# Kernel optimization log

Hardware: AMD Instinct MI355X
Metric: run time of the kernel (lower is better)

Reference implementation:

```python
import jax, jax.numpy as jnp
import numpy as np

N_HEAD = 8
N_FEAT = 512
D_HEAD = N_FEAT // N_HEAD


def setup_inputs() -> dict:
    key = jax.random.key(0)
    ks = jax.random.split(key, 11)
    B, T, L = 4, 2048, 16
    s = 1.0 / np.sqrt(D_HEAD)
    so = 1.0 / np.sqrt(N_FEAT)
    return {
        "q": jax.random.normal(ks[0], (B, T, 1, N_FEAT), jnp.float32),
        "k": jax.random.normal(ks[1], (B, T, L, N_FEAT), jnp.float32),
        "v": jax.random.normal(ks[2], (B, T, L, N_FEAT), jnp.float32),
        "Wq": jax.random.uniform(ks[3], (D_HEAD, D_HEAD), jnp.float32, -s, s),
        "bq": jax.random.uniform(ks[4], (D_HEAD,), jnp.float32, -s, s),
        "Wk": jax.random.uniform(ks[5], (D_HEAD, D_HEAD), jnp.float32, -s, s),
        "bk": jax.random.uniform(ks[6], (D_HEAD,), jnp.float32, -s, s),
        "Wv": jax.random.uniform(ks[7], (D_HEAD, D_HEAD), jnp.float32, -s, s),
        "bv": jax.random.uniform(ks[8], (D_HEAD,), jnp.float32, -s, s),
        "Wo": jax.random.uniform(ks[9], (N_FEAT, N_FEAT), jnp.float32, -so, so),
        "bo": jax.random.uniform(ks[10], (N_FEAT,), jnp.float32, -so, so),
    }


def reference(q, k, v, Wq, bq, Wk, bk, Wv, bv, Wo, bo):
    B, T, L, F = k.shape
    H, D = N_HEAD, D_HEAD
    # split heads: q [B,T,H,D] (query axis of length 1 squeezed), k/v [B,T,L,H,D]
    qh = q.reshape(B, T, H, D)
    kh = k.reshape(B, T, L, H, D)
    vh = v.reshape(B, T, L, H, D)
    # per-head linear projections (shared across heads), Linear: x @ W^T + b
    qh = jnp.einsum("bthd,ed->bthe", qh, Wq) + bq
    kh = jnp.einsum("btlhd,ed->btlhe", kh, Wk) + bk
    vh = jnp.einsum("btlhd,ed->btlhe", vh, Wv) + bv
    # attention scores over the local window L (query length 1 per timestep)
    attw = jnp.einsum("bthd,btlhd->bthl", qh, kh) / jnp.sqrt(jnp.asarray(D, qh.dtype))
    attn = jax.nn.softmax(attw, axis=-1)  # dropout is identity in eval mode
    ct = jnp.einsum("bthl,btlhd->bthd", attn, vh)
    ct = ct.reshape(B, T, F)
    return ct @ Wo.T + bo
```

## Files before the change

kernel.cpp:

```cpp
#include <hip/hip_runtime.h>


#define NFEAT 512
#define NHEAD 8
#define DHEAD 64
#define LWIN  16
#define WPOS  8
#define FBT   16
#define VPITCH 520

typedef __attribute__((ext_vector_type(8))) short bf16x8;
typedef __attribute__((ext_vector_type(4))) float f32x4;

__device__ __forceinline__ unsigned short f2bf(float f) {
    unsigned int u = __float_as_uint(f);
    unsigned int r = (u + 0x7fffu + ((u >> 16) & 1u)) >> 16;
    return (unsigned short)r;
}

__global__ void precompute_small(const float* __restrict__ Wq, const float* __restrict__ bq,
                                 const float* __restrict__ Wk,
                                 const float* __restrict__ Wo, const float* __restrict__ bo,
                                 const float* __restrict__ bv,
                                 float* __restrict__ A, float* __restrict__ g,
                                 float* __restrict__ b2) {
    int idx = blockIdx.x * 256 + threadIdx.x;
    if (idx < 4096) {
        int d = idx >> 6, dp = idx & 63;
        float s = 0.f;
        #pragma unroll 8
        for (int e = 0; e < 64; ++e) s = fmaf(Wq[e * 64 + d], Wk[e * 64 + dp], s);
        A[idx] = s;
    } else if (idx < 4160) {
        int dp = idx - 4096;
        float s = 0.f;
        #pragma unroll 8
        for (int e = 0; e < 64; ++e) s = fmaf(Wk[e * 64 + dp], bq[e], s);
        g[dp] = s;
    } else if (idx < 4672) {
        int j = idx - 4160;
        float s = bo[j];
        #pragma unroll 8
        for (int i = 0; i < 512; ++i) s = fmaf(Wo[j * 512 + i], bv[i & 63], s);
        b2[j] = s;
    }
}

__global__ void precompute_wo2(const float* __restrict__ Wo, const float* __restrict__ Wv,
                               unsigned short* __restrict__ Wo2B) {
    int idx = blockIdx.x * 256 + threadIdx.x;
    int i = idx & 511, j = idx >> 9;
    int h = i >> 6, e = i & 63;
    float s = 0.f;
    #pragma unroll 8
    for (int d = 0; d < 64; ++d)
        s = fmaf(Wo[j * 512 + h * 64 + d], Wv[d * 64 + e], s);
    Wo2B[(size_t)j * 512 + i] = f2bf(s);
}

__global__ __launch_bounds__(512, 4)
void w_prepass(const float* __restrict__ q, const float* __restrict__ A,
               const float* __restrict__ g, float* __restrict__ Wm) {
    __shared__ float As[4096];
    __shared__ float qs[WPOS][NFEAT];
    const int tid = threadIdx.x;
    const int bt0 = blockIdx.x * WPOS;

    #pragma unroll
    for (int i = 0; i < 8; ++i) As[i * 512 + tid] = A[i * 512 + tid];
    #pragma unroll
    for (int r = 0; r < WPOS; ++r) qs[r][tid] = q[(size_t)(bt0 + r) * NFEAT + tid];
    __syncthreads();

    const int e  = tid & 63;
    const int hb = (tid >> 6) << 6;
    float acc[WPOS];
    const float ge = g[e];
    #pragma unroll
    for (int r = 0; r < WPOS; ++r) acc[r] = ge;

    #pragma unroll 4
    for (int dq = 0; dq < 16; ++dq) {
        const float a0 = As[(4 * dq + 0) * 64 + e];
        const float a1 = As[(4 * dq + 1) * 64 + e];
        const float a2 = As[(4 * dq + 2) * 64 + e];
        const float a3 = As[(4 * dq + 3) * 64 + e];
        #pragma unroll
        for (int r = 0; r < WPOS; ++r) {
            const float4 qv = *reinterpret_cast<const float4*>(&qs[r][hb + 4 * dq]);
            acc[r] = fmaf(qv.x, a0, acc[r]);
            acc[r] = fmaf(qv.y, a1, acc[r]);
            acc[r] = fmaf(qv.z, a2, acc[r]);
            acc[r] = fmaf(qv.w, a3, acc[r]);
        }
    }
    #pragma unroll
    for (int r = 0; r < WPOS; ++r)
        Wm[(size_t)(bt0 + r) * NFEAT + tid] = acc[r] * 0.125f;
}

__global__ __launch_bounds__(512, 4)
void attn_fused(const float* __restrict__ Wm, const float* __restrict__ k,
                const float* __restrict__ v, const unsigned short* __restrict__ Wo2B,
                const float* __restrict__ b2, float* __restrict__ out) {
    __shared__ float ps[NHEAD][FBT][17];
    __shared__ __align__(16) unsigned char uni[FBT * NFEAT * 4];
    float*          wsT   = reinterpret_cast<float*>(uni);
    unsigned short* vbarS = reinterpret_cast<unsigned short*>(uni);

    const int tid = threadIdx.x;
    const int bt0 = blockIdx.x * FBT;

    #pragma unroll 4
    for (int r = 0; r < FBT; ++r)
        wsT[r * NFEAT + tid] = Wm[(size_t)(bt0 + r) * NFEAT + tid];
    __syncthreads();

    {
        const int h    = tid >> 6;
        const int lane = tid & 63;
        const int l    = lane >> 2;
        const int d4   = lane & 3;
        #pragma unroll 4
        for (int pp = 0; pp < FBT; ++pp) {
            const float4* w4 = reinterpret_cast<const float4*>(
                wsT + pp * NFEAT + h * 64 + d4 * 16);
            const float4* k4 = reinterpret_cast<const float4*>(
                k + (size_t)(bt0 + pp) * (LWIN * NFEAT) + (size_t)l * NFEAT + h * 64 + d4 * 16);
            float a0 = 0.f, a1 = 0.f, a2 = 0.f, a3 = 0.f;
            #pragma unroll
            for (int i = 0; i < 4; ++i) {
                const float4 wq = w4[i];
                const float4 kq = k4[i];
                a0 = fmaf(wq.x, kq.x, a0);
                a1 = fmaf(wq.y, kq.y, a1);
                a2 = fmaf(wq.z, kq.z, a2);
                a3 = fmaf(wq.w, kq.w, a3);
            }
            float sc = (a0 + a1) + (a2 + a3);
            sc += __shfl_xor(sc, 1, 64);
            sc += __shfl_xor(sc, 2, 64);
            const float e = __expf(sc);
            float s = e;
            s += __shfl_xor(s, 4, 64);
            s += __shfl_xor(s, 8, 64);
            s += __shfl_xor(s, 16, 64);
            s += __shfl_xor(s, 32, 64);
            if (d4 == 0) ps[h][pp][l] = e * (1.0f / s);
        }
    }
    __syncthreads();

    {
        const int pb = tid >> 7;
        const int f4 = tid & 127;
        const int hh = f4 >> 4;
        #pragma unroll
        for (int ii = 0; ii < 4; ++ii) {
            const int bt = ii * 4 + pb;
            float pv[LWIN];
            #pragma unroll
            for (int i = 0; i < LWIN; ++i) pv[i] = ps[hh][bt][i];
            const float4* vp = reinterpret_cast<const float4*>(
                v + (size_t)(bt0 + bt) * (LWIN * NFEAT)) + f4;
            float ax = 0.f, ay = 0.f, az = 0.f, aw = 0.f;
            #pragma unroll
            for (int l = 0; l < LWIN; ++l) {
                const float4 vv = vp[(size_t)l * 128];
                ax = fmaf(pv[l], vv.x, ax);
                ay = fmaf(pv[l], vv.y, ay);
                az = fmaf(pv[l], vv.z, az);
                aw = fmaf(pv[l], vv.w, aw);
            }
            unsigned short o[4] = { f2bf(ax), f2bf(ay), f2bf(az), f2bf(aw) };
            *reinterpret_cast<uint2*>(vbarS + bt * VPITCH + f4 * 4) =
                *reinterpret_cast<uint2*>(o);
        }
    }
    __syncthreads();

    {
        const int w    = tid >> 6;
        const int lane = tid & 63;
        const int n0   = w * 64;
        const int r    = lane & 15;
        const int kg   = lane >> 4;

        const unsigned short* As0 = vbarS + r * VPITCH + kg * 8;
        const short* Bb0 = (const short*)Wo2B + ((size_t)(n0 +  0 + r)) * 512 + kg * 8;
        const short* Bb1 = (const short*)Wo2B + ((size_t)(n0 + 16 + r)) * 512 + kg * 8;
        const short* Bb2 = (const short*)Wo2B + ((size_t)(n0 + 32 + r)) * 512 + kg * 8;
        const short* Bb3 = (const short*)Wo2B + ((size_t)(n0 + 48 + r)) * 512 + kg * 8;

        f32x4 acc0 = {0.f, 0.f, 0.f, 0.f}, acc1 = acc0, acc2 = acc0, acc3 = acc0;

        #pragma unroll 4
        for (int kk = 0; kk < 16; ++kk) {
            const bf16x8 a   = *reinterpret_cast<const bf16x8*>(As0 + kk * 32);
            const bf16x8 b0  = *reinterpret_cast<const bf16x8*>(Bb0 + kk * 32);
            const bf16x8 b1  = *reinterpret_cast<const bf16x8*>(Bb1 + kk * 32);
            const bf16x8 b2v = *reinterpret_cast<const bf16x8*>(Bb2 + kk * 32);
            const bf16x8 b3  = *reinterpret_cast<const bf16x8*>(Bb3 + kk * 32);
            acc0 = __builtin_amdgcn_mfma_f32_16x16x32_bf16(a, b0,  acc0, 0, 0, 0);
            acc1 = __builtin_amdgcn_mfma_f32_16x16x32_bf16(a, b1,  acc1, 0, 0, 0);
            acc2 = __builtin_amdgcn_mfma_f32_16x16x32_bf16(a, b2v, acc2, 0, 0, 0);
            acc3 = __builtin_amdgcn_mfma_f32_16x16x32_bf16(a, b3,  acc3, 0, 0, 0);
        }

        const float bb0 = b2[n0 + 0 + r],  bb1 = b2[n0 + 16 + r];
        const float bb2 = b2[n0 + 32 + r], bb3 = b2[n0 + 48 + r];
        #pragma unroll
        for (int j = 0; j < 4; ++j) {
            const size_t row = (size_t)(bt0 + kg * 4 + j) * 512;
            out[row + n0 +  0 + r] = acc0[j] + bb0;
            out[row + n0 + 16 + r] = acc1[j] + bb1;
            out[row + n0 + 32 + r] = acc2[j] + bb2;
            out[row + n0 + 48 + r] = acc3[j] + bb3;
        }
    }
}

extern "C" void kernel_launch(void* const* d_in, const int* in_sizes, int n_in,
                              void* d_out, int out_size, void* d_ws, size_t ws_size,
                              hipStream_t stream) {
    const float* q  = (const float*)d_in[0];
    const float* k  = (const float*)d_in[1];
    const float* v  = (const float*)d_in[2];
    const float* Wq = (const float*)d_in[3];
    const float* bq = (const float*)d_in[4];
    const float* Wk = (const float*)d_in[5];
    const float* Wv = (const float*)d_in[7];
    const float* bv = (const float*)d_in[8];
    const float* Wo = (const float*)d_in[9];
    const float* bo = (const float*)d_in[10];
    float* out = (float*)d_out;

    float* ws = (float*)d_ws;
    float*          A    = ws;
    float*          g    = ws + 4096;
    float*          b2   = ws + 4160;
    unsigned short* Wo2B = (unsigned short*)(ws + 4672);
    float*          Wm   = ws + 4672 + 131072;

    const int BT = in_sizes[0] / NFEAT;

    hipLaunchKernelGGL(precompute_small, dim3(19), dim3(256), 0, stream,
                       Wq, bq, Wk, Wo, bo, bv, A, g, b2);
    hipLaunchKernelGGL(precompute_wo2, dim3(1024), dim3(256), 0, stream,
                       Wo, Wv, Wo2B);
    hipLaunchKernelGGL(w_prepass, dim3(BT / WPOS), dim3(512), 0, stream,
                       q, A, g, Wm);
    hipLaunchKernelGGL(attn_fused, dim3(BT / FBT), dim3(512), 0, stream,
                       Wm, k, v, Wo2B, b2, out);
}
```

Baseline: 174.9 us.

## Read Wm directly from global and batch loads ahead of FMAs with sched barriers

Drops the LDS staging of the Wm tile and its barrier, reading the per-position query-projected weights straight from global memory in the score phase. Scores are now processed two timesteps at a time, and both the score and V-weighting phases issue all their global loads before a sched_barrier, so more memory requests are in flight before the arithmetic starts. This removes a shared-memory round trip and one sync and shrinks LDS use to the bf16 vbar buffer only. In exchange, register pressure rises under the 512-thread, 4-block launch bound, which can lead to spills, and the outer V loop is no longer unrolled.

```diff
diff --git a/kernel.cpp b/kernel.cpp
--- a/kernel.cpp
+++ b/kernel.cpp
@@ -99,79 +99,133 @@
         Wm[(size_t)(bt0 + r) * NFEAT + tid] = acc[r] * 0.125f;
 }
 
+__device__ __forceinline__ void dot4x4(const float4 w0, const float4 w1,
+                                       const float4 w2, const float4 w3,
+                                       const float4 k0, const float4 k1,
+                                       const float4 k2, const float4 k3,
+                                       float& outv) {
+    float a0 = 0.f, a1 = 0.f, a2 = 0.f, a3 = 0.f;
+    a0 = fmaf(w0.x, k0.x, a0); a1 = fmaf(w0.y, k0.y, a1);
+    a2 = fmaf(w0.z, k0.z, a2); a3 = fmaf(w0.w, k0.w, a3);
+    a0 = fmaf(w1.x, k1.x, a0); a1 = fmaf(w1.y, k1.y, a1);
+    a2 = fmaf(w1.z, k1.z, a2); a3 = fmaf(w1.w, k1.w, a3);
+    a0 = fmaf(w2.x, k2.x, a0); a1 = fmaf(w2.y, k2.y, a1);
+    a2 = fmaf(w2.z, k2.z, a2); a3 = fmaf(w2.w, k2.w, a3);
+    a0 = fmaf(w3.x, k3.x, a0); a1 = fmaf(w3.y, k3.y, a1);
+    a2 = fmaf(w3.z, k3.z, a2); a3 = fmaf(w3.w, k3.w, a3);
+    outv = (a0 + a1) + (a2 + a3);
+}
+
 __global__ __launch_bounds__(512, 4)
 void attn_fused(const float* __restrict__ Wm, const float* __restrict__ k,
                 const float* __restrict__ v, const unsigned short* __restrict__ Wo2B,
                 const float* __restrict__ b2, float* __restrict__ out) {
     __shared__ float ps[NHEAD][FBT][17];
-    __shared__ __align__(16) unsigned char uni[FBT * NFEAT * 4];
-    float*          wsT   = reinterpret_cast<float*>(uni);
-    unsigned short* vbarS = reinterpret_cast<unsigned short*>(uni);
+    __shared__ __align__(16) unsigned short vbarS[FBT * VPITCH];
 
     const int tid = threadIdx.x;
     const int bt0 = blockIdx.x * FBT;
-
-    #pragma unroll 4
-    for (int r = 0; r < FBT; ++r)
-        wsT[r * NFEAT + tid] = Wm[(size_t)(bt0 + r) * NFEAT + tid];
-    __syncthreads();
 
     {
         const int h    = tid >> 6;
         const int lane = tid & 63;
         const int l    = lane >> 2;
         const int d4   = lane & 3;
-        #pragma unroll 4
-        for (int pp = 0; pp < FBT; ++pp) {
-            const float4* w4 = reinterpret_cast<const float4*>(
-                wsT + pp * NFEAT + h * 64 + d4 * 16);
-            const float4* k4 = reinterpret_cast<const float4*>(
-                k + (size_t)(bt0 + pp) * (LWIN * NFEAT) + (size_t)l * NFEAT + h * 64 + d4 * 16);
-            float a0 = 0.f, a1 = 0.f, a2 = 0.f, a3 = 0.f;
-            #pragma unroll
-            for (int i = 0; i < 4; ++i) {
-                const float4 wq = w4[i];
-                const float4 kq = k4[i];
-                a0 = fmaf(wq.x, kq.x, a0);
-                a1 = fmaf(wq.y, kq.y, a1);
-                a2 = fmaf(wq.z, kq.z, a2);
-                a3 = fmaf(wq.w, kq.w, a3);
+        const int off  = h * 64 + d4 * 16;
+
+        for (int pp2 = 0; pp2 < FBT / 2; ++pp2) {
+            const int pa = 2 * pp2, pb = 2 * pp2 + 1;
+            const float4* wA = reinterpret_cast<const float4*>(
+                Wm + (size_t)(bt0 + pa) * NFEAT + off);
+            const float4* wB = reinterpret_cast<const float4*>(
+                Wm + (size_t)(bt0 + pb) * NFEAT + off);
+            const float4* kA = reinterpret_cast<const float4*>(
+                k + (size_t)(bt0 + pa) * (LWIN * NFEAT) + (size_t)l * NFEAT + off);
+            const float4* kB = reinterpret_cast<const float4*>(
+                k + (size_t)(bt0 + pb) * (LWIN * NFEAT) + (size_t)l * NFEAT + off);
+
+            const float4 wa0 = wA[0], wa1 = wA[1], wa2 = wA[2], wa3 = wA[3];
+            const float4 ka0 = kA[0], ka1 = kA[1], ka2 = kA[2], ka3 = kA[3];
+            const float4 wb0 = wB[0], wb1 = wB[1], wb2 = wB[2], wb3 = wB[3];
+            const float4 kb0 = kB[0], kb1 = kB[1], kb2 = kB[2], kb3 = kB[3];
+            __builtin_amdgcn_sched_barrier(0);
+
+            float sa, sb;
+            dot4x4(wa0, wa1, wa2, wa3, ka0, ka1, ka2, ka3, sa);
+            dot4x4(wb0, wb1, wb2, wb3, kb0, kb1, kb2, kb3, sb);
+
+            sa += __shfl_xor(sa, 1, 64);  sb += __shfl_xor(sb, 1, 64);
+            sa += __shfl_xor(sa, 2, 64);  sb += __shfl_xor(sb, 2, 64);
+            const float ea = __expf(sa);  const float eb = __expf(sb);
+            float da = ea, db = eb;
+            da += __shfl_xor(da, 4, 64);  db += __shfl_xor(db, 4, 64);
+            da += __shfl_xor(da, 8, 64);  db += __shfl_xor(db, 8, 64);
+            da += __shfl_xor(da, 16, 64); db += __shfl_xor(db, 16, 64);
+            da += __shfl_xor(da, 32, 64); db += __shfl_xor(db, 32, 64);
+            if (d4 == 0) {
+                ps[h][pa][l] = ea * (1.0f / da);
+                ps[h][pb][l] = eb * (1.0f / db);
             }
-            float sc = (a0 + a1) + (a2 + a3);
-            sc += __shfl_xor(sc, 1, 64);
-            sc += __shfl_xor(sc, 2, 64);
-            const float e = __expf(sc);
-            float s = e;
-            s += __shfl_xor(s, 4, 64);
-            s += __shfl_xor(s, 8, 64);
-            s += __shfl_xor(s, 16, 64);
-            s += __shfl_xor(s, 32, 64);
-            if (d4 == 0) ps[h][pp][l] = e * (1.0f / s);
         }
     }
     __syncthreads();
 
     {
-        const int pb = tid >> 7;
+        const int pq = tid >> 7;
         const int f4 = tid & 127;
         const int hh = f4 >> 4;
-        #pragma unroll
         for (int ii = 0; ii < 4; ++ii) {
-            const int bt = ii * 4 + pb;
+            const int bt = ii * 4 + pq;
             float pv[LWIN];
             #pragma unroll
             for (int i = 0; i < LWIN; ++i) pv[i] = ps[hh][bt][i];
             const float4* vp = reinterpret_cast<const float4*>(
                 v + (size_t)(bt0 + bt) * (LWIN * NFEAT)) + f4;
+
+            const float4 x0  = vp[ 0 * 128], x1  = vp[ 1 * 128];
+            const float4 x2  = vp[ 2 * 128], x3  = vp[ 3 * 128];
+            const float4 x4  = vp[ 4 * 128], x5  = vp[ 5 * 128];
+            const float4 x6  = vp[ 6 * 128], x7  = vp[ 7 * 128];
+            const float4 x8  = vp[ 8 * 128], x9  = vp[ 9 * 128];
+            const float4 x10 = vp[10 * 128], x11 = vp[11 * 128];
+            const float4 x12 = vp[12 * 128], x13 = vp[13 * 128];
+            const float4 x14 = vp[14 * 128], x15 = vp[15 * 128];
+            __builtin_amdgcn_sched_barrier(0);
+
             float ax = 0.f, ay = 0.f, az = 0.f, aw = 0.f;
-            #pragma unroll
-            for (int l = 0; l < LWIN; ++l) {
-                const float4 vv = vp[(size_t)l * 128];
-                ax = fmaf(pv[l], vv.x, ax);
-                ay = fmaf(pv[l], vv.y, ay);
-                az = fmaf(pv[l], vv.z, az);
-                aw = fmaf(pv[l], vv.w, aw);
-            }
+            ax = fmaf(pv[ 0], x0.x,  ax); ay = fmaf(pv[ 0], x0.y,  ay);
+            az = fmaf(pv[ 0], x0.z,  az); aw = fmaf(pv[ 0], x0.w,  aw);
+            ax = fmaf(pv[ 1], x1.x,  ax); ay = fmaf(pv[ 1], x1.y,  ay);
+            az = fmaf(pv[ 1], x1.z,  az); aw = fmaf(pv[ 1], x1.w,  aw);
+            ax = fmaf(pv[ 2], x2.x,  ax); ay = fmaf(pv[ 2], x2.y,  ay);
+            az = fmaf(pv[ 2], x2.z,  az); aw = fmaf(pv[ 2], x2.w,  aw);
+            ax = fmaf(pv[ 3], x3.x,  ax); ay = fmaf(pv[ 3], x3.y,  ay);
+            az = fmaf(pv[ 3], x3.z,  az); aw = fmaf(pv[ 3], x3.w,  aw);
+            ax = fmaf(pv[ 4], x4.x,  ax); ay = fmaf(pv[ 4], x4.y,  ay);
+            az = fmaf(pv[ 4], x4.z,  az); aw = fmaf(pv[ 4], x4.w,  aw);
+            ax = fmaf(pv[ 5], x5.x,  ax); ay = fmaf(pv[ 5], x5.y,  ay);
+            az = fmaf(pv[ 5], x5.z,  az); aw = fmaf(pv[ 5], x5.w,  aw);
+            ax = fmaf(pv[ 6], x6.x,  ax); ay = fmaf(pv[ 6], x6.y,  ay);
+            az = fmaf(pv[ 6], x6.z,  az); aw = fmaf(pv[ 6], x6.w,  aw);
+            ax = fmaf(pv[ 7], x7.x,  ax); ay = fmaf(pv[ 7], x7.y,  ay);
+            az = fmaf(pv[ 7], x7.z,  az); aw = fmaf(pv[ 7], x7.w,  aw);
+            ax = fmaf(pv[ 8], x8.x,  ax); ay = fmaf(pv[ 8], x8.y,  ay);
+            az = fmaf(pv[ 8], x8.z,  az); aw = fmaf(pv[ 8], x8.w,  aw);
+            ax = fmaf(pv[ 9], x9.x,  ax); ay = fmaf(pv[ 9], x9.y,  ay);
+            az = fmaf(pv[ 9], x9.z,  az); aw = fmaf(pv[ 9], x9.w,  aw);
+            ax = fmaf(pv[10], x10.x, ax); ay = fmaf(pv[10], x10.y, ay);
+            az = fmaf(pv[10], x10.z, az); aw = fmaf(pv[10], x10.w, aw);
+            ax = fmaf(pv[11], x11.x, ax); ay = fmaf(pv[11], x11.y, ay);
+            az = fmaf(pv[11], x11.z, az); aw = fmaf(pv[11], x11.w, aw);
+            ax = fmaf(pv[12], x12.x, ax); ay = fmaf(pv[12], x12.y, ay);
+            az = fmaf(pv[12], x12.z, az); aw = fmaf(pv[12], x12.w, aw);
+            ax = fmaf(pv[13], x13.x, ax); ay = fmaf(pv[13], x13.y, ay);
+            az = fmaf(pv[13], x13.z, az); aw = fmaf(pv[13], x13.w, aw);
+            ax = fmaf(pv[14], x14.x, ax); ay = fmaf(pv[14], x14.y, ay);
+            az = fmaf(pv[14], x14.z, az); aw = fmaf(pv[14], x14.w, aw);
+            ax = fmaf(pv[15], x15.x, ax); ay = fmaf(pv[15], x15.y, ay);
+            az = fmaf(pv[15], x15.z, az); aw = fmaf(pv[15], x15.w, aw);
+
             unsigned short o[4] = { f2bf(ax), f2bf(ay), f2bf(az), f2bf(aw) };
             *reinterpret_cast<uint2*>(vbarS + bt * VPITCH + f4 * 4) =
                 *reinterpret_cast<uint2*>(o);
```

New measurement: 181.2 us. +3.6%, slower.

## Halve rows per block, drop Wm LDS staging, defer softmax normalization

Applied to the files above, without the earlier changes.

Cuts the timesteps per block from 16 to 8 and removes the shared-memory staging of the projected query rows, which are now read straight from global memory. This shrinks LDS use so the launch bound can ask for 8 blocks per CU. The softmax sum is no longer a cross-lane shuffle reduction; it is computed per thread from the stored exponentials and applied after the value accumulation. The MFMA tile still uses 16 rows, so half its work is redundant (rows 8-15 duplicate 0-7) and those outputs are not stored, and the Wo weights are reloaded twice as often per output row.

```diff
diff --git a/kernel.cpp b/kernel.cpp
--- a/kernel.cpp
+++ b/kernel.cpp
@@ -6,7 +6,7 @@
 #define DHEAD 64
 #define LWIN  16
 #define WPOS  8
-#define FBT   16
+#define FBT   8
 #define VPITCH 520
 
 typedef __attribute__((ext_vector_type(8))) short bf16x8;
@@ -99,34 +99,28 @@
         Wm[(size_t)(bt0 + r) * NFEAT + tid] = acc[r] * 0.125f;
 }
 
-__global__ __launch_bounds__(512, 4)
+__global__ __launch_bounds__(512, 8)
 void attn_fused(const float* __restrict__ Wm, const float* __restrict__ k,
                 const float* __restrict__ v, const unsigned short* __restrict__ Wo2B,
                 const float* __restrict__ b2, float* __restrict__ out) {
     __shared__ float ps[NHEAD][FBT][17];
-    __shared__ __align__(16) unsigned char uni[FBT * NFEAT * 4];
-    float*          wsT   = reinterpret_cast<float*>(uni);
-    unsigned short* vbarS = reinterpret_cast<unsigned short*>(uni);
+    __shared__ __align__(16) unsigned short vbarS[FBT * VPITCH];
 
     const int tid = threadIdx.x;
     const int bt0 = blockIdx.x * FBT;
-
-    #pragma unroll 4
-    for (int r = 0; r < FBT; ++r)
-        wsT[r * NFEAT + tid] = Wm[(size_t)(bt0 + r) * NFEAT + tid];
-    __syncthreads();
 
     {
         const int h    = tid >> 6;
         const int lane = tid & 63;
         const int l    = lane >> 2;
         const int d4   = lane & 3;
-        #pragma unroll 4
-        for (int pp = 0; pp < FBT; ++pp) {
+        const int off  = h * 64 + d4 * 16;
+
+        for (int p = 0; p < FBT; ++p) {
             const float4* w4 = reinterpret_cast<const float4*>(
-                wsT + pp * NFEAT + h * 64 + d4 * 16);
+                Wm + (size_t)(bt0 + p) * NFEAT + off);
             const float4* k4 = reinterpret_cast<const float4*>(
-                k + (size_t)(bt0 + pp) * (LWIN * NFEAT) + (size_t)l * NFEAT + h * 64 + d4 * 16);
+                k + (size_t)(bt0 + p) * (LWIN * NFEAT) + (size_t)l * NFEAT + off);
             float a0 = 0.f, a1 = 0.f, a2 = 0.f, a3 = 0.f;
             #pragma unroll
             for (int i = 0; i < 4; ++i) {
@@ -141,26 +135,27 @@
             sc += __shfl_xor(sc, 1, 64);
             sc += __shfl_xor(sc, 2, 64);
             const float e = __expf(sc);
-            float s = e;
-            s += __shfl_xor(s, 4, 64);
-            s += __shfl_xor(s, 8, 64);
-            s += __shfl_xor(s, 16, 64);
-            s += __shfl_xor(s, 32, 64);
-            if (d4 == 0) ps[h][pp][l] = e * (1.0f / s);
+            if (d4 == 0) ps[h][p][l] = e;
         }
     }
     __syncthreads();
 
     {
-        const int pb = tid >> 7;
+        const int pq = tid >> 7;
         const int f4 = tid & 127;
         const int hh = f4 >> 4;
         #pragma unroll
-        for (int ii = 0; ii < 4; ++ii) {
-            const int bt = ii * 4 + pb;
+        for (int ii = 0; ii < FBT / 4; ++ii) {
+            const int bt = ii * 4 + pq;
             float pv[LWIN];
             #pragma unroll
             for (int i = 0; i < LWIN; ++i) pv[i] = ps[hh][bt][i];
+            float s0 = (pv[0] + pv[1]) + (pv[2] + pv[3]);
+            float s1 = (pv[4] + pv[5]) + (pv[6] + pv[7]);
+            float s2 = (pv[8] + pv[9]) + (pv[10] + pv[11]);
+            float s3 = (pv[12] + pv[13]) + (pv[14] + pv[15]);
+            const float inv = 1.0f / ((s0 + s1) + (s2 + s3));
+
             const float4* vp = reinterpret_cast<const float4*>(
                 v + (size_t)(bt0 + bt) * (LWIN * NFEAT)) + f4;
             float ax = 0.f, ay = 0.f, az = 0.f, aw = 0.f;
@@ -172,6 +167,7 @@
                 az = fmaf(pv[l], vv.z, az);
                 aw = fmaf(pv[l], vv.w, aw);
             }
+            ax *= inv; ay *= inv; az *= inv; aw *= inv;
             unsigned short o[4] = { f2bf(ax), f2bf(ay), f2bf(az), f2bf(aw) };
             *reinterpret_cast<uint2*>(vbarS + bt * VPITCH + f4 * 4) =
                 *reinterpret_cast<uint2*>(o);
@@ -186,7 +182,7 @@
         const int r    = lane & 15;
         const int kg   = lane >> 4;
 
-        const unsigned short* As0 = vbarS + r * VPITCH + kg * 8;
+        const unsigned short* As0 = vbarS + (r & 7) * VPITCH + kg * 8;
         const short* Bb0 = (const short*)Wo2B + ((size_t)(n0 +  0 + r)) * 512 + kg * 8;
         const short* Bb1 = (const short*)Wo2B + ((size_t)(n0 + 16 + r)) * 512 + kg * 8;
         const short* Bb2 = (const short*)Wo2B + ((size_t)(n0 + 32 + r)) * 512 + kg * 8;
@@ -207,15 +203,17 @@
             acc3 = __builtin_amdgcn_mfma_f32_16x16x32_bf16(a, b3,  acc3, 0, 0, 0);
         }
 
-        const float bb0 = b2[n0 + 0 + r],  bb1 = b2[n0 + 16 + r];
-        const float bb2 = b2[n0 + 32 + r], bb3 = b2[n0 + 48 + r];
-        #pragma unroll
-        for (int j = 0; j < 4; ++j) {
-            const size_t row = (size_t)(bt0 + kg * 4 + j) * 512;
-            out[row + n0 +  0 + r] = acc0[j] + bb0;
-            out[row + n0 + 16 + r] = acc1[j] + bb1;
-            out[row + n0 + 32 + r] = acc2[j] + bb2;
-            out[row + n0 + 48 + r] = acc3[j] + bb3;
+        if (kg < 2) {
+            const float bb0 = b2[n0 + 0 + r],  bb1 = b2[n0 + 16 + r];
+            const float bb2 = b2[n0 + 32 + r], bb3 = b2[n0 + 48 + r];
+            #pragma unroll
+            for (int j = 0; j < 4; ++j) {
+                const size_t row = (size_t)(bt0 + kg * 4 + j) * 512;
+                out[row + n0 +  0 + r] = acc0[j] + bb0;
+                out[row + n0 + 16 + r] = acc1[j] + bb1;
+                out[row + n0 + 32 + r] = acc2[j] + bb2;
+                out[row + n0 + 48 + r] = acc3[j] + bb3;
+            }
         }
     }
 }
```

After: 209.7 us. +19.9%, slower.
